# Kernel optimization log

Hardware: AMD Instinct MI355X
Metric: run time of the kernel (lower is better)

## Reference

```python
import jax, jax.numpy as jnp
import numpy as np

ALPHA, BETA, GAMMA, DELTA = 0.3, 0.3, 0.2, 0.2
BK, BW = 3, 3.0
EPS = 1e-7


def _bce_with_logits(x, y):
    # numerically stable: max(x,0) - x*y + log(1+exp(-|x|)); pos_weight=1.0
    return jnp.maximum(x, 0.0) - x * y + jnp.log1p(jnp.exp(-jnp.abs(x)))


def _lovasz_hinge_flat(x, y):
    # x, y: (N,) flattened logits / binary labels for one image
    signs = 2.0 * y - 1.0
    errors = 1.0 - x * signs
    perm = jnp.argsort(-errors)            # descending sort permutation
    errors_sorted = errors[perm]
    gt_sorted = y[perm]
    gts = gt_sorted.sum()
    intersection = gts - jnp.cumsum(gt_sorted)
    union = gts + jnp.cumsum(1.0 - gt_sorted)
    jaccard = 1.0 - intersection / union
    jaccard = jnp.concatenate([jaccard[:1], jaccard[1:] - jaccard[:-1]])
    return jnp.dot(jax.nn.relu(errors_sorted), jaccard)


def setup_inputs() -> dict:
    key = jax.random.key(0)
    k1, k2 = jax.random.split(key)
    logits = jax.random.normal(k1, (32, 1, 512, 512), dtype=jnp.float32)
    # binary ground-truth mask (0/1 floats)
    targets = jnp.round(jax.random.uniform(k2, (32, 1, 512, 512), dtype=jnp.float32))
    return {"logits": logits, "targets": targets}


def reference(logits, targets):
    # --- BCE term (pos_weight = 1.0) ---
    bce_elem = _bce_with_logits(logits, targets)
    bce = bce_elem.mean()

    # --- Dice term ---
    probs = jax.nn.sigmoid(logits)
    num = 2.0 * (probs * targets).sum(axis=(2, 3))
    den = (probs + targets).sum(axis=(2, 3)) + EPS
    dice = 1.0 - (num / den).mean()

    # --- Boundary-weighted BCE term (weights computed under no_grad) ---
    kernel = jnp.ones((1, 1, BK, BK), logits.dtype) / (BK * BK)
    smooth = jax.lax.conv_general_dilated(
        targets, kernel, window_strides=(1, 1), padding='SAME',
        dimension_numbers=('NCHW', 'OIHW', 'NCHW'))
    edges = ((smooth > 0.01) & (smooth < 0.99)).astype(logits.dtype)
    weights = jax.lax.stop_gradient(1.0 + edges * (BW - 1.0))
    boundary = (bce_elem * weights).mean()

    # --- Lovasz hinge, per image then averaged ---
    B = logits.shape[0]
    lov = jax.vmap(_lovasz_hinge_flat)(
        logits.reshape(B, -1), targets.reshape(B, -1)).mean()

    return ALPHA * bce + BETA * dice + GAMMA * boundary + DELTA * lov
```

## Files before the change

kernel.cpp:

```cpp
#include <hip/hip_runtime.h>
#include <hip/hip_bf16.h>


#define NB      32
#define HH      512
#define WW      512
#define HW      (HH*WW)
#define NTOT    (NB*HW)
#define K_BINS  1024
#define INV_H   128.0f
#define BIN_W   (1.0f/128.0f)

struct Ws {
    unsigned cnt[NB*K_BINS];
    float    sy[NB];
    float    spy[NB];
    float    Pim[NB];
    float    bce_sum;
    float    bceE_sum;
    float    lov_sum;
};

__device__ __forceinline__ void process_elem(float x, float y, float wsum,
                                             float& bce_s, float& bceE_s, float& sy_s,
                                             float& spy_s, float& P_s,
                                             unsigned* s_cnt) {
    const float ax = fabsf(x);
    const float t  = __expf(-ax);
    const float bce = fmaxf(x, 0.f) - x * y + __logf(1.f + t);
    const float inv = __builtin_amdgcn_rcpf(1.f + t);
    const float s = (x >= 0.f) ? inv : t * inv;
    const bool edge = (wsum > 0.5f) && (wsum < 8.5f);

    bce_s  += bce;
    bceE_s += edge ? bce : 0.f;
    sy_s   += s * y;
    spy_s  += s + y;
    P_s    += y;

    const float e = 1.f - x * (2.f * y - 1.f);
    if (e > 0.f) {
        int b = (int)(e * INV_H);
        if (b > K_BINS - 1) b = K_BINS - 1;
        atomicAdd(&s_cnt[b], (y > 0.5f) ? 0x10001u : 1u);
    }
}

__global__ __launch_bounds__(256, 2) void kernelA(const float* __restrict__ logits,
                                                  const float* __restrict__ targets,
                                                  Ws* __restrict__ ws) {
    __shared__ unsigned s_cnt[K_BINS];
    __shared__ float    red[4][5];

    const int tid  = threadIdx.x;
    const int lane = tid & 63;
    const int wave = tid >> 6;
    for (int i = tid; i < K_BINS; i += 256) s_cnt[i] = 0u;
    __syncthreads();

    const int img   = blockIdx.x >> 4;
    const int strip = ((blockIdx.x & 15) << 2) | wave;
    const int r0    = strip * 8;

    const float4* __restrict__ tg4 = (const float4*)(targets + img * HW);
    const float4* __restrict__ lg4 = (const float4*)(logits  + img * HW);
    const int cA = lane;
    const int cB = 64 + lane;

    float4 T[5][2]; float fT[5];
    float4 X[3][2];

#pragma unroll
    for (int s = 0; s < 5; ++s) {
        const int rr = r0 - 1 + s;
        const int rc = rr < 0 ? 0 : (rr > 511 ? 511 : rr);
        fT[s] = (rr >= 0 && rr < 512) ? 1.f : 0.f;
        T[s][0] = tg4[rc * 128 + cA];
        T[s][1] = tg4[rc * 128 + cB];
    }
#pragma unroll
    for (int s = 0; s < 3; ++s) {
        const int rr = r0 + s;
        X[s][0] = lg4[rr * 128 + cA];
        X[s][1] = lg4[rr * 128 + cB];
    }

    float bce_s = 0.f, bceE_s = 0.f, sy_s = 0.f, spy_s = 0.f, P_s = 0.f;

#pragma unroll
    for (int j = 0; j < 8; ++j) {
        const int ia = j % 5, ib = (j + 1) % 5, ic = (j + 2) % 5;
        const int xs = j % 3;
        const float fa = fT[ia], fc = fT[ic];

        float4 csA, csB;
        csA.x = fmaf(T[ia][0].x, fa, fmaf(T[ic][0].x, fc, T[ib][0].x));
        csA.y = fmaf(T[ia][0].y, fa, fmaf(T[ic][0].y, fc, T[ib][0].y));
        csA.z = fmaf(T[ia][0].z, fa, fmaf(T[ic][0].z, fc, T[ib][0].z));
        csA.w = fmaf(T[ia][0].w, fa, fmaf(T[ic][0].w, fc, T[ib][0].w));
        csB.x = fmaf(T[ia][1].x, fa, fmaf(T[ic][1].x, fc, T[ib][1].x));
        csB.y = fmaf(T[ia][1].y, fa, fmaf(T[ic][1].y, fc, T[ib][1].y));
        csB.z = fmaf(T[ia][1].z, fa, fmaf(T[ic][1].z, fc, T[ib][1].z));
        csB.w = fmaf(T[ia][1].w, fa, fmaf(T[ic][1].w, fc, T[ib][1].w));

        const float upA  = __shfl_up(csA.w, 1);
        const float dnA  = __shfl_down(csA.x, 1);
        const float upB  = __shfl_up(csB.w, 1);
        const float dnB  = __shfl_down(csB.x, 1);
        const float bc0  = __shfl(csB.x, 0);
        const float bc63 = __shfl(csA.w, 63);
        const float LA = (lane == 0)  ? 0.f  : upA;
        const float RA = (lane == 63) ? bc0  : dnA;
        const float LB = (lane == 0)  ? bc63 : upB;
        const float RB = (lane == 63) ? 0.f  : dnB;

        process_elem(X[xs][0].x, T[ib][0].x, LA + csA.x + csA.y,    bce_s, bceE_s, sy_s, spy_s, P_s, s_cnt);
        process_elem(X[xs][0].y, T[ib][0].y, csA.x + csA.y + csA.z, bce_s, bceE_s, sy_s, spy_s, P_s, s_cnt);
        process_elem(X[xs][0].z, T[ib][0].z, csA.y + csA.z + csA.w, bce_s, bceE_s, sy_s, spy_s, P_s, s_cnt);
        process_elem(X[xs][0].w, T[ib][0].w, csA.z + csA.w + RA,    bce_s, bceE_s, sy_s, spy_s, P_s, s_cnt);
        process_elem(X[xs][1].x, T[ib][1].x, LB + csB.x + csB.y,    bce_s, bceE_s, sy_s, spy_s, P_s, s_cnt);
        process_elem(X[xs][1].y, T[ib][1].y, csB.x + csB.y + csB.z, bce_s, bceE_s, sy_s, spy_s, P_s, s_cnt);
        process_elem(X[xs][1].z, T[ib][1].z, csB.y + csB.z + csB.w, bce_s, bceE_s, sy_s, spy_s, P_s, s_cnt);
        process_elem(X[xs][1].w, T[ib][1].w, csB.z + csB.w + RB,    bce_s, bceE_s, sy_s, spy_s, P_s, s_cnt);

        if (j < 5) {
            const int rr = r0 + j + 4;
            const int rc = rr > 511 ? 511 : rr;
            fT[ia] = (rr < 512) ? 1.f : 0.f;
            T[ia][0] = tg4[rc * 128 + cA];
            T[ia][1] = tg4[rc * 128 + cB];
            const int rx = r0 + j + 3;
            X[xs][0] = lg4[rx * 128 + cA];
            X[xs][1] = lg4[rx * 128 + cB];
        }
    }
    __syncthreads();

    unsigned* g_c = ws->cnt + img * K_BINS;
    for (int i = tid; i < K_BINS; i += 256) {
        const unsigned cpk = s_cnt[i];
        if (cpk) atomicAdd(&g_c[i], cpk);
    }

    for (int off = 32; off; off >>= 1) {
        bce_s  += __shfl_down(bce_s, off);
        bceE_s += __shfl_down(bceE_s, off);
        sy_s   += __shfl_down(sy_s, off);
        spy_s  += __shfl_down(spy_s, off);
        P_s    += __shfl_down(P_s, off);
    }
    if (lane == 0) {
        red[wave][0] = bce_s; red[wave][1] = bceE_s; red[wave][2] = sy_s;
        red[wave][3] = spy_s; red[wave][4] = P_s;
    }
    __syncthreads();
    if (tid == 0) {
        float a = 0.f, b = 0.f, c2 = 0.f, d = 0.f, e2 = 0.f;
        for (int w = 0; w < 4; ++w) {
            a += red[w][0]; b += red[w][1]; c2 += red[w][2];
            d += red[w][3]; e2 += red[w][4];
        }
        atomicAdd(&ws->bce_sum, a);
        atomicAdd(&ws->bceE_sum, b);
        atomicAdd(&ws->sy[img], c2);
        atomicAdd(&ws->spy[img], d);
        atomicAdd(&ws->Pim[img], e2);
    }
}

__global__ __launch_bounds__(256) void kernelB(Ws* __restrict__ ws) {
    __shared__ unsigned sc_a[256];
    __shared__ unsigned sc_p[256];
    __shared__ double   dred[4];

    const int img = blockIdx.x;
    const int tid = threadIdx.x;
    const unsigned* __restrict__ cn = ws->cnt + img * K_BINS;

    unsigned la[4], lp[4];
    float    me[4];
    unsigned tot_a = 0, tot_p = 0;
#pragma unroll
    for (int j = 0; j < 4; ++j) {
        const int k = K_BINS - 1 - (tid * 4 + j);
        const unsigned cpk = cn[k];
        la[j] = cpk & 0xFFFFu; lp[j] = cpk >> 16;
        me[j] = ((float)k + 0.5f) * BIN_W;
        tot_a += la[j]; tot_p += lp[j];
    }

    sc_a[tid] = tot_a; sc_p[tid] = tot_p;
    __syncthreads();
    for (int off = 1; off < 256; off <<= 1) {
        unsigned va = (tid >= off) ? sc_a[tid - off] : 0u;
        unsigned vp = (tid >= off) ? sc_p[tid - off] : 0u;
        __syncthreads();
        sc_a[tid] += va; sc_p[tid] += vp;
        __syncthreads();
    }
    const unsigned excl_a = sc_a[tid] - tot_a;
    const unsigned excl_p = sc_p[tid] - tot_p;

    const double P = (double)ws->Pim[img];
    double run_a = (double)excl_a, run_p = (double)excl_p;
    double contrib = 0.0;
#pragma unroll
    for (int j = 0; j < 4; ++j) {
        const double m = (double)la[j];
        const double p = (double)lp[j];
        if (la[j]) {
            const double u = P + (run_a + 0.5 * m) - (run_p + 0.5 * p);
            const double c = run_p + 0.5 * p;
            contrib += (double)(lp[j] * me[j]) / u;
            const double den = u * (u - 1.0);
            if (den > 0.0)
                contrib += (double)((la[j] - lp[j]) * me[j]) * (P - c) / den;
        }
        run_a += m; run_p += p;
    }

    for (int off = 32; off; off >>= 1) contrib += __shfl_down(contrib, off);
    const int wave = tid >> 6;
    const int lane = tid & 63;
    if (lane == 0) dred[wave] = contrib;
    __syncthreads();
    if (tid == 0) {
        double tot = dred[0] + dred[1] + dred[2] + dred[3];
        atomicAdd(&ws->lov_sum, (float)tot);
    }
}

__global__ __launch_bounds__(64) void kernelC(const Ws* __restrict__ ws,
                                              float* __restrict__ out) {
    const int lane = threadIdx.x;
    float dsum = 0.f;
    if (lane < NB) {
        const float num = 2.f * ws->sy[lane];
        const float den = ws->spy[lane] + 1e-7f;
        dsum = num / den;
    }
    for (int off = 32; off; off >>= 1) dsum += __shfl_down(dsum, off);
    if (lane == 0) {
        const float invN = 1.f / (float)NTOT;
        const float bce      = ws->bce_sum * invN;
        const float boundary = (ws->bce_sum + 2.f * ws->bceE_sum) * invN;
        const float dice     = 1.f - dsum / (float)NB;
        const float lov      = ws->lov_sum / (float)NB;
        out[0] = 0.3f * bce + 0.3f * dice + 0.2f * boundary + 0.2f * lov;
    }
}

extern "C" void kernel_launch(void* const* d_in, const int* in_sizes, int n_in,
                              void* d_out, int out_size, void* d_ws, size_t ws_size,
                              hipStream_t stream) {
    const float* logits  = (const float*)d_in[0];
    const float* targets = (const float*)d_in[1];
    float* out = (float*)d_out;
    Ws* ws = (Ws*)d_ws;

    (void)hipMemsetAsync(d_ws, 0, sizeof(Ws), stream);
    kernelA<<<NB * 16, 256, 0, stream>>>(logits, targets, ws);
    kernelB<<<NB, 256, 0, stream>>>(ws);
    kernelC<<<1, 64, 0, stream>>>(ws, out);
}
```

Measured before the change: 116.1 us.

## Fuse histogram scan and final reduction into main kernel via last-block pattern

Merges the per-image Lovasz scan kernel and the final combine kernel into the main streaming kernel. Per-image and global completion counters let the last block of each image, and then the last image, run the scan and write the output. This removes two kernel launches and their gaps between dependent launches. In exchange the main kernel uses more shared memory and adds threadfences and atomic reads, which could lower occupancy.

After: 117.8 us. No clear change (+1.5%).

```diff
diff --git a/kernel.cpp b/kernel.cpp
--- a/kernel.cpp
+++ b/kernel.cpp
@@ -19,6 +19,8 @@
     float    bce_sum;
     float    bceE_sum;
     float    lov_sum;
+    unsigned blkdone[NB];
+    unsigned imgdone;
 };
 
 __device__ __forceinline__ void process_elem(float x, float y, float wsum,
@@ -48,9 +50,14 @@
 
 __global__ __launch_bounds__(256, 2) void kernelA(const float* __restrict__ logits,
                                                   const float* __restrict__ targets,
-                                                  Ws* __restrict__ ws) {
+                                                  Ws* __restrict__ ws,
+                                                  float* __restrict__ out) {
     __shared__ unsigned s_cnt[K_BINS];
     __shared__ float    red[4][5];
+    __shared__ unsigned sc_a[256];
+    __shared__ unsigned sc_p[256];
+    __shared__ double   dred[4];
+    __shared__ unsigned s_flag, s_flag2;
 
     const int tid  = threadIdx.x;
     const int lane = tid & 63;
@@ -165,88 +172,89 @@
         atomicAdd(&ws->sy[img], c2);
         atomicAdd(&ws->spy[img], d);
         atomicAdd(&ws->Pim[img], e2);
-    }
-}
-
-__global__ __launch_bounds__(256) void kernelB(Ws* __restrict__ ws) {
-    __shared__ unsigned sc_a[256];
-    __shared__ unsigned sc_p[256];
-    __shared__ double   dred[4];
-
-    const int img = blockIdx.x;
-    const int tid = threadIdx.x;
-    const unsigned* __restrict__ cn = ws->cnt + img * K_BINS;
-
-    unsigned la[4], lp[4];
-    float    me[4];
-    unsigned tot_a = 0, tot_p = 0;
-#pragma unroll
-    for (int j = 0; j < 4; ++j) {
-        const int k = K_BINS - 1 - (tid * 4 + j);
-        const unsigned cpk = cn[k];
-        la[j] = cpk & 0xFFFFu; lp[j] = cpk >> 16;
-        me[j] = ((float)k + 0.5f) * BIN_W;
-        tot_a += la[j]; tot_p += lp[j];
-    }
-
-    sc_a[tid] = tot_a; sc_p[tid] = tot_p;
-    __syncthreads();
-    for (int off = 1; off < 256; off <<= 1) {
-        unsigned va = (tid >= off) ? sc_a[tid - off] : 0u;
-        unsigned vp = (tid >= off) ? sc_p[tid - off] : 0u;
+        __threadfence();
+        const unsigned d16 = atomicAdd(&ws->blkdone[img], 1u);
+        s_flag = (d16 == 15u) ? 1u : 0u;
+    }
+    __syncthreads();
+
+    if (s_flag) {
+        unsigned* cn = ws->cnt + img * K_BINS;
+
+        unsigned la[4], lp[4];
+        float    me[4];
+        unsigned tot_a = 0, tot_p = 0;
+#pragma unroll
+        for (int j = 0; j < 4; ++j) {
+            const int k = K_BINS - 1 - (tid * 4 + j);
+            const unsigned cpk = atomicAdd(&cn[k], 0u);
+            la[j] = cpk & 0xFFFFu; lp[j] = cpk >> 16;
+            me[j] = ((float)k + 0.5f) * BIN_W;
+            tot_a += la[j]; tot_p += lp[j];
+        }
+
+        sc_a[tid] = tot_a; sc_p[tid] = tot_p;
         __syncthreads();
-        sc_a[tid] += va; sc_p[tid] += vp;
+        for (int off = 1; off < 256; off <<= 1) {
+            unsigned va = (tid >= off) ? sc_a[tid - off] : 0u;
+            unsigned vp = (tid >= off) ? sc_p[tid - off] : 0u;
+            __syncthreads();
+            sc_a[tid] += va; sc_p[tid] += vp;
+            __syncthreads();
+        }
+        const unsigned excl_a = sc_a[tid] - tot_a;
+        const unsigned excl_p = sc_p[tid] - tot_p;
+
+        const double P = (double)atomicAdd(&ws->Pim[img], 0.f);
+        double run_a = (double)excl_a, run_p = (double)excl_p;
+        double contrib = 0.0;
+#pragma unroll
+        for (int j = 0; j < 4; ++j) {
+            const double m = (double)la[j];
+            const double p = (double)lp[j];
+            if (la[j]) {
+                const double u = P + (run_a + 0.5 * m) - (run_p + 0.5 * p);
+                const double c = run_p + 0.5 * p;
+                contrib += (double)(lp[j] * me[j]) / u;
+                const double den = u * (u - 1.0);
+                if (den > 0.0)
+                    contrib += (double)((la[j] - lp[j]) * me[j]) * (P - c) / den;
+            }
+            run_a += m; run_p += p;
+        }
+
+        for (int off = 32; off; off >>= 1) contrib += __shfl_down(contrib, off);
+        if (lane == 0) dred[wave] = contrib;
         __syncthreads();
-    }
-    const unsigned excl_a = sc_a[tid] - tot_a;
-    const unsigned excl_p = sc_p[tid] - tot_p;
-
-    const double P = (double)ws->Pim[img];
-    double run_a = (double)excl_a, run_p = (double)excl_p;
-    double contrib = 0.0;
-#pragma unroll
-    for (int j = 0; j < 4; ++j) {
-        const double m = (double)la[j];
-        const double p = (double)lp[j];
-        if (la[j]) {
-            const double u = P + (run_a + 0.5 * m) - (run_p + 0.5 * p);
-            const double c = run_p + 0.5 * p;
-            contrib += (double)(lp[j] * me[j]) / u;
-            const double den = u * (u - 1.0);
-            if (den > 0.0)
-                contrib += (double)((la[j] - lp[j]) * me[j]) * (P - c) / den;
-        }
-        run_a += m; run_p += p;
-    }
-
-    for (int off = 32; off; off >>= 1) contrib += __shfl_down(contrib, off);
-    const int wave = tid >> 6;
-    const int lane = tid & 63;
-    if (lane == 0) dred[wave] = contrib;
-    __syncthreads();
-    if (tid == 0) {
-        double tot = dred[0] + dred[1] + dred[2] + dred[3];
-        atomicAdd(&ws->lov_sum, (float)tot);
-    }
-}
-
-__global__ __launch_bounds__(64) void kernelC(const Ws* __restrict__ ws,
-                                              float* __restrict__ out) {
-    const int lane = threadIdx.x;
-    float dsum = 0.f;
-    if (lane < NB) {
-        const float num = 2.f * ws->sy[lane];
-        const float den = ws->spy[lane] + 1e-7f;
-        dsum = num / den;
-    }
-    for (int off = 32; off; off >>= 1) dsum += __shfl_down(dsum, off);
-    if (lane == 0) {
-        const float invN = 1.f / (float)NTOT;
-        const float bce      = ws->bce_sum * invN;
-        const float boundary = (ws->bce_sum + 2.f * ws->bceE_sum) * invN;
-        const float dice     = 1.f - dsum / (float)NB;
-        const float lov      = ws->lov_sum / (float)NB;
-        out[0] = 0.3f * bce + 0.3f * dice + 0.2f * boundary + 0.2f * lov;
+        if (tid == 0) {
+            const double tot = dred[0] + dred[1] + dred[2] + dred[3];
+            atomicAdd(&ws->lov_sum, (float)tot);
+            __threadfence();
+            const unsigned d32 = atomicAdd(&ws->imgdone, 1u);
+            s_flag2 = (d32 == (unsigned)(NB - 1)) ? 1u : 0u;
+        }
+        __syncthreads();
+
+        if (s_flag2 && wave == 0) {
+            float dsum = 0.f;
+            if (lane < NB) {
+                const float syv  = atomicAdd(&ws->sy[lane], 0.f);
+                const float spyv = atomicAdd(&ws->spy[lane], 0.f);
+                dsum = 2.f * syv / (spyv + 1e-7f);
+            }
+            for (int off = 32; off; off >>= 1) dsum += __shfl_down(dsum, off);
+            if (lane == 0) {
+                const float bsum = atomicAdd(&ws->bce_sum, 0.f);
+                const float besm = atomicAdd(&ws->bceE_sum, 0.f);
+                const float lsum = atomicAdd(&ws->lov_sum, 0.f);
+                const float invN = 1.f / (float)NTOT;
+                const float bce      = bsum * invN;
+                const float boundary = (bsum + 2.f * besm) * invN;
+                const float dice     = 1.f - dsum / (float)NB;
+                const float lov      = lsum / (float)NB;
+                out[0] = 0.3f * bce + 0.3f * dice + 0.2f * boundary + 0.2f * lov;
+            }
+        }
     }
 }
 
@@ -259,7 +267,5 @@
     Ws* ws = (Ws*)d_ws;
 
     (void)hipMemsetAsync(d_ws, 0, sizeof(Ws), stream);
-    kernelA<<<NB * 16, 256, 0, stream>>>(logits, targets, ws);
-    kernelB<<<NB, 256, 0, stream>>>(ws);
-    kernelC<<<1, 64, 0, stream>>>(ws, out);
+    kernelA<<<NB * 16, 256, 0, stream>>>(logits, targets, ws, out);
 }
```
